# Kernel optimization log

Measured on AMD Instinct MI355X. Metric: run time of the kernel, lower is better.

## Reference

```python
import jax, jax.numpy as jnp
import numpy as np

R = 16
ALPHA = 32.0
SCALING = ALPHA / R


def setup_inputs() -> dict:
    key = jax.random.key(0)
    ks = jax.random.split(key, 6)
    B, T, C, O, E = 16, 1500, 1024, 1024, 8
    x = jax.random.normal(ks[0], (B, T, C), dtype=jnp.float32)
    # gate weights per batch element (e.g. softmax-like, but module accepts any)
    w = jax.random.uniform(ks[1], (B, E), dtype=jnp.float32)
    W_base = jax.random.normal(ks[2], (O, C), dtype=jnp.float32) * 0.02
    b_base = jax.random.normal(ks[3], (O,), dtype=jnp.float32) * 0.02
    As = jax.random.normal(ks[4], (E, R, C), dtype=jnp.float32) * 0.02
    Bs = jax.random.normal(ks[5], (E, O, R), dtype=jnp.float32) * 0.02
    return {"x": x, "w": w, "W_base": W_base, "b_base": b_base, "As": As, "Bs": Bs}


def reference(x, w, W_base, b_base, As, Bs):
    # base linear: (B,T,C) @ (C,O) + b
    out = jnp.einsum('btc,oc->bto', x, W_base) + b_base
    # per-expert low-rank: h[b,t,e,r] = x[b,t,:] @ A_e^T
    h = jnp.einsum('btc,erc->bter', x, As)          # (B,T,E,R)
    # y[b,t,e,o] = h @ B_e^T ; gate-weighted sum over experts
    lora = jnp.einsum('bter,eor,be->bto', h, Bs, w)  # (B,T,O)
    return out + lora * SCALING
```

## Files before the change

kernel.cpp:

```cpp
#include <hip/hip_runtime.h>
#include <stdint.h>
#include <stddef.h>


#define B_ 16
#define T_ 1500
#define C_ 1024
#define O_ 1024
#define E_ 8
#define R_ 16
#define ER 128
#define KK 1152
#define BT 24000
#define NKT 18
#define SCALING 2.0f

typedef __bf16 bf16x8 __attribute__((ext_vector_type(8)));
typedef float f32x4 __attribute__((ext_vector_type(4)));
typedef unsigned short u16;
typedef u16 u16x8 __attribute__((ext_vector_type(8)));

__device__ inline u16 f2bf(float f) {
  union { float f; unsigned u; } v; v.f = f;
  unsigned u = v.u;
  u += 0x7fff + ((u >> 16) & 1);
  return (u16)(u >> 16);
}

#define GLL(gp, lp)                                                            \
  __builtin_amdgcn_global_load_lds(                                            \
      (const __attribute__((address_space(1))) void*)(gp),                     \
      (__attribute__((address_space(3))) void*)(lp), 16, 0, 0)

__global__ __launch_bounds__(256) void prep_w(const float* __restrict__ Wb,
                                              const float* __restrict__ Bs,
                                              const float* __restrict__ As,
                                              u16* __restrict__ wp,
                                              u16* __restrict__ ap) {
  int idx = blockIdx.x * 256 + threadIdx.x;
  if (idx < O_ * KK) {
    int o = idx / KK;
    int k = idx - o * KK;
    float v;
    if (k < C_) {
      v = Wb[o * C_ + k];
    } else {
      int j = k - C_;
      v = Bs[((j >> 4) * O_ + o) * R_ + (j & 15)];
    }
    wp[idx] = f2bf(v);
  } else {
    int a = idx - O_ * KK;
    ap[a] = f2bf(As[a]);
  }
}

__global__ __launch_bounds__(256) void cvt(const float* __restrict__ x,
                                           u16* __restrict__ xp) {
  const int t0 = blockIdx.x * 256 + threadIdx.x;
#pragma unroll
  for (int u = 0; u < 6; ++u) {
    const int chunk = u * 512000 + t0;
    const int row = chunk >> 7;
    const int cc = (chunk & 127) * 8;
    const float4 v0 = *(const float4*)&x[(size_t)row * C_ + cc];
    const float4 v1 = *(const float4*)&x[(size_t)row * C_ + cc + 4];
    u16x8 o;
    o[0] = f2bf(v0.x); o[1] = f2bf(v0.y); o[2] = f2bf(v0.z); o[3] = f2bf(v0.w);
    o[4] = f2bf(v1.x); o[5] = f2bf(v1.y); o[6] = f2bf(v1.z); o[7] = f2bf(v1.w);
    *(u16x8*)&xp[(size_t)row * KK + cc] = o;
  }
}

__global__ __launch_bounds__(256) void h_gemm(const u16* __restrict__ xp,
                                              const u16* __restrict__ ab,
                                              const float* __restrict__ w,
                                              u16* __restrict__ xpo) {
  const int mt = blockIdx.x;
  const int tid = threadIdx.x, lane = tid & 63, wv = tid >> 6;
  const int wrow = wv & 1, wcol = wv >> 1, l15 = lane & 15, quad = lane >> 4;
  const int s7 = l15 & 7;

  __shared__ u16 lA[64 * 64];
  __shared__ u16 lB[128 * 64];

  const u16* gA = xp + (size_t)mt * 64 * KK;

  f32x4 acc[2][4];
#pragma unroll
  for (int i = 0; i < 2; ++i)
#pragma unroll
    for (int j = 0; j < 4; ++j) acc[i][j] = (f32x4){0.f, 0.f, 0.f, 0.f};

  int arow[2], ako[2], brow[4], bko[4];
#pragma unroll
  for (int c = 0; c < 2; ++c) {
    int idx = c * 256 + tid;
    arow[c] = idx >> 3;
    ako[c] = (((idx & 7) ^ (arow[c] & 7)) << 3);
  }
#pragma unroll
  for (int c = 0; c < 4; ++c) {
    int idx = c * 256 + tid;
    brow[c] = idx >> 3;
    bko[c] = (((idx & 7) ^ (brow[c] & 7)) << 3);
  }

  for (int kt = 0; kt < C_ / 64; ++kt) {
    const int k0 = kt * 64;
#pragma unroll
    for (int c = 0; c < 2; ++c)
      GLL(gA + (size_t)arow[c] * KK + k0 + ako[c], &lA[(c * 256 + tid) * 8]);
#pragma unroll
    for (int c = 0; c < 4; ++c)
      GLL(ab + brow[c] * C_ + k0 + bko[c], &lB[(c * 256 + tid) * 8]);
    __syncthreads();
#pragma unroll
    for (int kk = 0; kk < 2; ++kk) {
      const int ko = (((kk * 4 + quad) ^ s7) << 3);
      bf16x8 af[2], bfr[4];
#pragma unroll
      for (int i = 0; i < 2; ++i)
        af[i] = *(const bf16x8*)&lA[(wrow * 32 + i * 16 + l15) * 64 + ko];
#pragma unroll
      for (int j = 0; j < 4; ++j)
        bfr[j] = *(const bf16x8*)&lB[(wcol * 64 + j * 16 + l15) * 64 + ko];
#pragma unroll
      for (int i = 0; i < 2; ++i)
#pragma unroll
        for (int j = 0; j < 4; ++j)
          acc[i][j] = __builtin_amdgcn_mfma_f32_16x16x32_bf16(af[i], bfr[j], acc[i][j], 0, 0, 0);
    }
    __syncthreads();
  }

#pragma unroll
  for (int j = 0; j < 4; ++j) {
    const int col = wcol * 64 + j * 16 + l15;
    const int e = wcol * 4 + j;
#pragma unroll
    for (int i = 0; i < 2; ++i) {
#pragma unroll
      for (int rr = 0; rr < 4; ++rr) {
        const int row = mt * 64 + wrow * 32 + i * 16 + quad * 4 + rr;
        const int b = row / T_;
        xpo[(size_t)row * KK + C_ + col] = f2bf(acc[i][j][rr] * (SCALING * w[b * E_ + e]));
      }
    }
  }
}

__global__ __launch_bounds__(256, 2) void main_gemm(const u16* __restrict__ xp,
                                                    const u16* __restrict__ wp,
                                                    const float* __restrict__ bb,
                                                    float* __restrict__ out) {
  const int id = blockIdx.x;
  const int g = (id & 7) * 188 + (id >> 3);
  const int mt = g >> 3;
  const int nt = g & 7;
  const int tid = threadIdx.x, lane = tid & 63, wv = tid >> 6;
  const int wm = wv >> 1, wn = wv & 1, l15 = lane & 15, quad = lane >> 4;
  const int s7 = l15 & 7;

  __shared__ u16 lA[2][128 * 64];
  __shared__ u16 lB[2][128 * 64];

  const u16* gA = xp + (size_t)mt * 128 * KK;
  const u16* gB = wp + (size_t)nt * 128 * KK;

  f32x4 acc[4][4];
#pragma unroll
  for (int i = 0; i < 4; ++i)
#pragma unroll
    for (int j = 0; j < 4; ++j) acc[i][j] = (f32x4){0.f, 0.f, 0.f, 0.f};

  const u16* pA[4];
  const u16* pB[4];
  int dst[4];
#pragma unroll
  for (int c = 0; c < 4; ++c) {
    int idx = c * 256 + tid;
    int row = idx >> 3;
    int ko = (((idx & 7) ^ (row & 7)) << 3);
    pA[c] = gA + (size_t)row * KK + ko;
    pB[c] = gB + (size_t)row * KK + ko;
    dst[c] = idx * 8;
  }

#pragma unroll
  for (int c = 0; c < 4; ++c) GLL(pA[c], &lA[0][dst[c]]);
#pragma unroll
  for (int c = 0; c < 4; ++c) GLL(pB[c], &lB[0][dst[c]]);
#pragma unroll
  for (int c = 0; c < 4; ++c) GLL(pA[c] + 64, &lA[1][dst[c]]);
#pragma unroll
  for (int c = 0; c < 4; ++c) GLL(pB[c] + 64, &lB[1][dst[c]]);

#pragma unroll 2
  for (int t = 0; t < NKT; ++t) {
    const int cur = t & 1;
    if (t < NKT - 1) {
      asm volatile("s_waitcnt vmcnt(8)" ::: "memory");
    } else {
      asm volatile("s_waitcnt vmcnt(0)" ::: "memory");
    }
    __builtin_amdgcn_sched_barrier(0);
    __builtin_amdgcn_s_barrier();
    __builtin_amdgcn_sched_barrier(0);

    bf16x8 af[4][2], bfr[4][2];
#pragma unroll
    for (int ks = 0; ks < 2; ++ks) {
      const int ko = (((ks * 4 + quad) ^ s7) << 3);
#pragma unroll
      for (int i = 0; i < 4; ++i) {
        af[i][ks] = *(const bf16x8*)&lA[cur][(wm * 64 + i * 16 + l15) * 64 + ko];
        bfr[i][ks] = *(const bf16x8*)&lB[cur][(wn * 64 + i * 16 + l15) * 64 + ko];
      }
    }
    asm volatile("s_waitcnt lgkmcnt(0)" ::: "memory");
    __builtin_amdgcn_sched_barrier(0);
    __builtin_amdgcn_s_barrier();
    __builtin_amdgcn_sched_barrier(0);

    if (t + 2 < NKT) {
      const int k2 = (t + 2) * 64;
#pragma unroll
      for (int c = 0; c < 4; ++c) GLL(pA[c] + k2, &lA[cur][dst[c]]);
#pragma unroll
      for (int c = 0; c < 4; ++c) GLL(pB[c] + k2, &lB[cur][dst[c]]);
    }

    __builtin_amdgcn_s_setprio(1);
#pragma unroll
    for (int ks = 0; ks < 2; ++ks)
#pragma unroll
      for (int i = 0; i < 4; ++i)
#pragma unroll
        for (int j = 0; j < 4; ++j)
          acc[i][j] = __builtin_amdgcn_mfma_f32_16x16x32_bf16(af[i][ks], bfr[j][ks],
                                                              acc[i][j], 0, 0, 0);
    __builtin_amdgcn_s_setprio(0);
  }

#pragma unroll
  for (int j = 0; j < 4; ++j) {
    const int col = nt * 128 + wn * 64 + j * 16 + l15;
    const float bias = bb[col];
#pragma unroll
    for (int i = 0; i < 4; ++i) {
#pragma unroll
      for (int rr = 0; rr < 4; ++rr) {
        const int row = mt * 128 + wm * 64 + i * 16 + quad * 4 + rr;
        if (row < BT) out[(size_t)row * O_ + col] = acc[i][j][rr] + bias;
      }
    }
  }
}

extern "C" void kernel_launch(void* const* d_in, const int* in_sizes, int n_in,
                              void* d_out, int out_size, void* d_ws, size_t ws_size,
                              hipStream_t stream) {
  const float* x = (const float*)d_in[0];
  const float* w = (const float*)d_in[1];
  const float* Wb = (const float*)d_in[2];
  const float* bb = (const float*)d_in[3];
  const float* As = (const float*)d_in[4];
  const float* Bs = (const float*)d_in[5];
  float* out = (float*)d_out;

  u16* xp = (u16*)d_ws;
  u16* wp = xp + (size_t)BT * KK;
  u16* ap = wp + (size_t)O_ * KK;

  prep_w<<<(O_ * KK + ER * C_) / 256, 256, 0, stream>>>(Wb, Bs, As, wp, ap);
  cvt<<<2000, 256, 0, stream>>>(x, xp);
  h_gemm<<<375, 256, 0, stream>>>(xp, ap, w, xp);
  main_gemm<<<1504, 256, 0, stream>>>(xp, wp, bb, out);
}
```

Baseline: 290.4 us.

## Enlarge main GEMM tile to 256x128 with 8 waves and split LDS-read/MFMA phases

The main GEMM block tile grows from 128x128 to 256x128 with 512 threads (8 waves in a 2x4 arrangement), halving the grid. Each wave now computes a 128x32 subtile. The inner loop is split so the first half of the A fragments is consumed by MFMAs while the second half is still loading from LDS, and the global prefetch is issued between the two halves. The goal is more reuse of each B tile and more overlap of LDS reads with matrix math, at the cost of more LDS per block (96KB) and possibly lower occupancy, since 2 blocks of 512 threads may not fit.

Result: no change. 292.0 us (+0.5%).

```diff
diff --git a/kernel.cpp b/kernel.cpp
--- a/kernel.cpp
+++ b/kernel.cpp
@@ -31,6 +31,8 @@
   __builtin_amdgcn_global_load_lds(                                            \
       (const __attribute__((address_space(1))) void*)(gp),                     \
       (__attribute__((address_space(3))) void*)(lp), 16, 0, 0)
+
+#define SBAR __builtin_amdgcn_sched_barrier(0)
 
 __global__ __launch_bounds__(256) void prep_w(const float* __restrict__ Wb,
                                               const float* __restrict__ Bs,
@@ -150,108 +152,132 @@
   }
 }
 
-__global__ __launch_bounds__(256, 2) void main_gemm(const u16* __restrict__ xp,
+__global__ __launch_bounds__(512, 2) void main_gemm(const u16* __restrict__ xp,
                                                     const u16* __restrict__ wp,
                                                     const float* __restrict__ bb,
                                                     float* __restrict__ out) {
   const int id = blockIdx.x;
-  const int g = (id & 7) * 188 + (id >> 3);
+  const int g = (id & 7) * 94 + (id >> 3);
   const int mt = g >> 3;
   const int nt = g & 7;
   const int tid = threadIdx.x, lane = tid & 63, wv = tid >> 6;
-  const int wm = wv >> 1, wn = wv & 1, l15 = lane & 15, quad = lane >> 4;
+  const int wm = wv >> 2, wn = wv & 3, l15 = lane & 15, quad = lane >> 4;
   const int s7 = l15 & 7;
 
-  __shared__ u16 lA[2][128 * 64];
+  __shared__ u16 lA[2][256 * 64];
   __shared__ u16 lB[2][128 * 64];
 
-  const u16* gA = xp + (size_t)mt * 128 * KK;
+  const u16* gA = xp + (size_t)mt * 256 * KK;
   const u16* gB = wp + (size_t)nt * 128 * KK;
 
-  f32x4 acc[4][4];
-#pragma unroll
-  for (int i = 0; i < 4; ++i)
-#pragma unroll
-    for (int j = 0; j < 4; ++j) acc[i][j] = (f32x4){0.f, 0.f, 0.f, 0.f};
+  f32x4 acc[8][2];
+#pragma unroll
+  for (int i = 0; i < 8; ++i)
+#pragma unroll
+    for (int j = 0; j < 2; ++j) acc[i][j] = (f32x4){0.f, 0.f, 0.f, 0.f};
 
   const u16* pA[4];
-  const u16* pB[4];
-  int dst[4];
+  const u16* pB[2];
+  int dA[4], dB[2];
 #pragma unroll
   for (int c = 0; c < 4; ++c) {
-    int idx = c * 256 + tid;
+    int idx = c * 512 + tid;
     int row = idx >> 3;
-    int ko = (((idx & 7) ^ (row & 7)) << 3);
-    pA[c] = gA + (size_t)row * KK + ko;
-    pB[c] = gB + (size_t)row * KK + ko;
-    dst[c] = idx * 8;
-  }
-
-#pragma unroll
-  for (int c = 0; c < 4; ++c) GLL(pA[c], &lA[0][dst[c]]);
-#pragma unroll
-  for (int c = 0; c < 4; ++c) GLL(pB[c], &lB[0][dst[c]]);
-#pragma unroll
-  for (int c = 0; c < 4; ++c) GLL(pA[c] + 64, &lA[1][dst[c]]);
-#pragma unroll
-  for (int c = 0; c < 4; ++c) GLL(pB[c] + 64, &lB[1][dst[c]]);
+    pA[c] = gA + (size_t)row * KK + (((idx & 7) ^ (row & 7)) << 3);
+    dA[c] = idx * 8;
+  }
+#pragma unroll
+  for (int c = 0; c < 2; ++c) {
+    int idx = c * 512 + tid;
+    int row = idx >> 3;
+    pB[c] = gB + (size_t)row * KK + (((idx & 7) ^ (row & 7)) << 3);
+    dB[c] = idx * 8;
+  }
+
+#pragma unroll
+  for (int c = 0; c < 4; ++c) GLL(pA[c], &lA[0][dA[c]]);
+#pragma unroll
+  for (int c = 0; c < 2; ++c) GLL(pB[c], &lB[0][dB[c]]);
+#pragma unroll
+  for (int c = 0; c < 4; ++c) GLL(pA[c] + 64, &lA[1][dA[c]]);
+#pragma unroll
+  for (int c = 0; c < 2; ++c) GLL(pB[c] + 64, &lB[1][dB[c]]);
 
 #pragma unroll 2
   for (int t = 0; t < NKT; ++t) {
     const int cur = t & 1;
     if (t < NKT - 1) {
-      asm volatile("s_waitcnt vmcnt(8)" ::: "memory");
+      asm volatile("s_waitcnt vmcnt(6)" ::: "memory");
     } else {
       asm volatile("s_waitcnt vmcnt(0)" ::: "memory");
     }
-    __builtin_amdgcn_sched_barrier(0);
+    SBAR;
     __builtin_amdgcn_s_barrier();
-    __builtin_amdgcn_sched_barrier(0);
-
-    bf16x8 af[4][2], bfr[4][2];
+    SBAR;
+
+    bf16x8 af0[4][2], af1[4][2], bfr[2][2];
 #pragma unroll
     for (int ks = 0; ks < 2; ++ks) {
       const int ko = (((ks * 4 + quad) ^ s7) << 3);
 #pragma unroll
-      for (int i = 0; i < 4; ++i) {
-        af[i][ks] = *(const bf16x8*)&lA[cur][(wm * 64 + i * 16 + l15) * 64 + ko];
-        bfr[i][ks] = *(const bf16x8*)&lB[cur][(wn * 64 + i * 16 + l15) * 64 + ko];
-      }
-    }
+      for (int i = 0; i < 4; ++i)
+        af0[i][ks] = *(const bf16x8*)&lA[cur][(wm * 128 + i * 16 + l15) * 64 + ko];
+#pragma unroll
+      for (int j = 0; j < 2; ++j)
+        bfr[j][ks] = *(const bf16x8*)&lB[cur][(wn * 32 + j * 16 + l15) * 64 + ko];
+    }
+    SBAR;
+#pragma unroll
+    for (int ks = 0; ks < 2; ++ks) {
+      const int ko = (((ks * 4 + quad) ^ s7) << 3);
+#pragma unroll
+      for (int i = 0; i < 4; ++i)
+        af1[i][ks] = *(const bf16x8*)&lA[cur][(wm * 128 + (i + 4) * 16 + l15) * 64 + ko];
+    }
+    asm volatile("s_waitcnt lgkmcnt(8)" ::: "memory");
+    SBAR;
+    __builtin_amdgcn_s_setprio(1);
+#pragma unroll
+    for (int ks = 0; ks < 2; ++ks)
+#pragma unroll
+      for (int i = 0; i < 4; ++i)
+#pragma unroll
+        for (int j = 0; j < 2; ++j)
+          acc[i][j] = __builtin_amdgcn_mfma_f32_16x16x32_bf16(af0[i][ks], bfr[j][ks],
+                                                              acc[i][j], 0, 0, 0);
+    __builtin_amdgcn_s_setprio(0);
     asm volatile("s_waitcnt lgkmcnt(0)" ::: "memory");
-    __builtin_amdgcn_sched_barrier(0);
+    SBAR;
     __builtin_amdgcn_s_barrier();
-    __builtin_amdgcn_sched_barrier(0);
-
+    SBAR;
     if (t + 2 < NKT) {
       const int k2 = (t + 2) * 64;
 #pragma unroll
-      for (int c = 0; c < 4; ++c) GLL(pA[c] + k2, &lA[cur][dst[c]]);
-#pragma unroll
-      for (int c = 0; c < 4; ++c) GLL(pB[c] + k2, &lB[cur][dst[c]]);
-    }
-
+      for (int c = 0; c < 4; ++c) GLL(pA[c] + k2, &lA[cur][dA[c]]);
+#pragma unroll
+      for (int c = 0; c < 2; ++c) GLL(pB[c] + k2, &lB[cur][dB[c]]);
+    }
     __builtin_amdgcn_s_setprio(1);
 #pragma unroll
     for (int ks = 0; ks < 2; ++ks)
 #pragma unroll
       for (int i = 0; i < 4; ++i)
 #pragma unroll
-        for (int j = 0; j < 4; ++j)
-          acc[i][j] = __builtin_amdgcn_mfma_f32_16x16x32_bf16(af[i][ks], bfr[j][ks],
-                                                              acc[i][j], 0, 0, 0);
+        for (int j = 0; j < 2; ++j)
+          acc[i + 4][j] = __builtin_amdgcn_mfma_f32_16x16x32_bf16(af1[i][ks], bfr[j][ks],
+                                                                  acc[i + 4][j], 0, 0, 0);
     __builtin_amdgcn_s_setprio(0);
   }
 
 #pragma unroll
-  for (int j = 0; j < 4; ++j) {
-    const int col = nt * 128 + wn * 64 + j * 16 + l15;
+  for (int j = 0; j < 2; ++j) {
+    const int col = nt * 128 + wn * 32 + j * 16 + l15;
     const float bias = bb[col];
 #pragma unroll
-    for (int i = 0; i < 4; ++i) {
+    for (int i = 0; i < 8; ++i) {
 #pragma unroll
       for (int rr = 0; rr < 4; ++rr) {
-        const int row = mt * 128 + wm * 64 + i * 16 + quad * 4 + rr;
+        const int row = mt * 256 + wm * 128 + i * 16 + quad * 4 + rr;
         if (row < BT) out[(size_t)row * O_ + col] = acc[i][j][rr] + bias;
       }
     }
@@ -276,5 +302,5 @@
   prep_w<<<(O_ * KK + ER * C_) / 256, 256, 0, stream>>>(Wb, Bs, As, wp, ap);
   cvt<<<2000, 256, 0, stream>>>(x, xp);
   h_gemm<<<375, 256, 0, stream>>>(xp, ap, w, xp);
-  main_gemm<<<1504, 256, 0, stream>>>(xp, wp, bb, out);
-}
+  main_gemm<<<752, 512, 0, stream>>>(xp, wp, bb, out);
+}
```
